# Performance work log

Hardware: AMD Instinct MI355X
Metric: run time of the kernel (lower is better)

Reference implementation:

```python
import jax, jax.numpy as jnp
import numpy as np

EMB = 1024
HEADS = 16
HEAD_DIM = EMB // HEADS
FF = 4 * EMB
B, S = 4, 2048


def gelu_tanh(x):
    c = jnp.sqrt(jnp.asarray(2.0 / jnp.pi, x.dtype))
    return 0.5 * x * (1.0 + jnp.tanh(c * (x + 0.044715 * x ** 3)))


def layernorm(x, g, b, eps=1e-5):
    mu = jnp.mean(x, axis=-1, keepdims=True)
    var = jnp.var(x, axis=-1, keepdims=True)
    return (x - mu) * jax.lax.rsqrt(var + eps) * g + b


def setup_inputs() -> dict:
    key = jax.random.key(0)
    ks = jax.random.split(key, 12)
    s = 0.02
    return {
        "x": jax.random.normal(ks[0], (B, S, EMB), jnp.float32),
        "Wq": jax.random.normal(ks[1], (EMB, EMB), jnp.float32) * s,
        "bq": jnp.zeros((EMB,), jnp.float32),
        "Wk": jax.random.normal(ks[2], (EMB, EMB), jnp.float32) * s,
        "bk": jnp.zeros((EMB,), jnp.float32),
        "Wv": jax.random.normal(ks[3], (EMB, EMB), jnp.float32) * s,
        "bv": jnp.zeros((EMB,), jnp.float32),
        "Wo": jax.random.normal(ks[4], (EMB, EMB), jnp.float32) * s,
        "bo": jnp.zeros((EMB,), jnp.float32),
        "W1": jax.random.normal(ks[5], (EMB, FF), jnp.float32) * s,
        "b1": jnp.zeros((FF,), jnp.float32),
        "W2": jax.random.normal(ks[6], (FF, EMB), jnp.float32) * s,
        "b2": jnp.zeros((EMB,), jnp.float32),
        "g1": jnp.ones((EMB,), jnp.float32),
        "be1": jnp.zeros((EMB,), jnp.float32),
        "g2": jnp.ones((EMB,), jnp.float32),
        "be2": jnp.zeros((EMB,), jnp.float32),
    }


def reference(x, Wq, bq, Wk, bk, Wv, bv, Wo, bo, W1, b1, W2, b2, g1, be1, g2, be2):
    b, s, _ = x.shape
    shortcut = x
    h = layernorm(x, g1, be1)
    # QKV projections -> [b, heads, s, head_dim]
    def proj(W, bias):
        return (h @ W + bias).reshape(b, s, HEADS, HEAD_DIM).transpose(0, 2, 1, 3)
    q, k, v = proj(Wq, bq), proj(Wk, bk), proj(Wv, bv)
    scores = jnp.einsum('bhqd,bhkd->bhqk', q, k) / jnp.sqrt(jnp.asarray(HEAD_DIM, x.dtype))
    causal = jnp.triu(jnp.ones((s, s), bool), k=1)  # True above diagonal -> masked
    scores = jnp.where(causal, -jnp.inf, scores)
    probs = jax.nn.softmax(scores, axis=-1)  # dropout p=0 -> identity
    ctx = jnp.einsum('bhqk,bhkd->bhqd', probs, v).transpose(0, 2, 1, 3).reshape(b, s, EMB)
    attn_out = ctx @ Wo + bo
    x = attn_out + shortcut
    shortcut = x
    h = layernorm(x, g2, be2)
    ff = gelu_tanh(h @ W1 + b1) @ W2 + b2
    return ff + shortcut
```

## Files before the change

### kernel.cpp

```cpp
#include <hip/hip_runtime.h>
#include <hip/hip_bf16.h>

#define EMB 1024
#define HEADS 16
#define HDIM 64
#define FFDIM 4096
#define BSZ 4
#define SEQ 2048
#define MROWS (BSZ * SEQ)
#define QKVW 3072
#define VSTRIDE 2080

typedef __attribute__((ext_vector_type(8))) short bf16x8;
typedef __attribute__((ext_vector_type(4))) float f32x4;
typedef __attribute__((ext_vector_type(16))) float f32x16;
typedef __attribute__((ext_vector_type(4))) unsigned short u16x4;
typedef unsigned short u16;

__device__ __forceinline__ float bf2f(u16 u) {
  union { unsigned int i; float f; } c; c.i = ((unsigned int)u) << 16; return c.f;
}
__device__ __forceinline__ u16 f2bf(float f) {
  union { float f; unsigned int i; } c; c.f = f;
  unsigned int i = c.i + 0x7fff + ((c.i >> 16) & 1);
  return (u16)(i >> 16);
}
__device__ __forceinline__ unsigned fbits(float f) {
  union { float f; unsigned u; } c; c.f = f; return c.u;
}
__device__ __forceinline__ unsigned pk2(float e0, float e1) {
  return (fbits(e0) >> 16) | (fbits(e1) & 0xffff0000u);
}
__device__ __forceinline__ f32x16 zero16() {
  f32x16 z;
#pragma unroll
  for (int i = 0; i < 16; ++i) z[i] = 0.f;
  return z;
}
__device__ __forceinline__ void gload16(const u16* g, void* lds) {
  __builtin_amdgcn_global_load_lds(
      (const __attribute__((address_space(1))) void*)g,
      (__attribute__((address_space(3))) void*)lds, 16, 0, 0);
}

__global__ __launch_bounds__(256) void ln_kernel(
    const float* __restrict__ x, const float* __restrict__ g,
    const float* __restrict__ be, u16* __restrict__ out) {
  int w = threadIdx.x >> 6, l = threadIdx.x & 63;
  size_t row = (size_t)blockIdx.x * 4 + w;
  const float* xr = x + row * EMB;
  float f[4][4];
  float s = 0.f, s2 = 0.f;
#pragma unroll
  for (int c = 0; c < 4; ++c) {
    f32x4 v = *(const f32x4*)(xr + c * 256 + l * 4);
#pragma unroll
    for (int j = 0; j < 4; ++j) {
      f[c][j] = v[j];
      s += v[j];
      s2 += v[j] * v[j];
    }
  }
#pragma unroll
  for (int m = 1; m < 64; m <<= 1) {
    s  += __shfl_xor(s, m);
    s2 += __shfl_xor(s2, m);
  }
  float mu = s * (1.f / EMB);
  float var = s2 * (1.f / EMB) - mu * mu;
  float rs = rsqrtf(var + 1e-5f);
#pragma unroll
  for (int c = 0; c < 4; ++c) {
    u16x4 o;
#pragma unroll
    for (int j = 0; j < 4; ++j) {
      int col = c * 256 + l * 4 + j;
      o[j] = f2bf((f[c][j] - mu) * rs * g[col] + be[col]);
    }
    *(u16x4*)(out + row * EMB + c * 256 + l * 4) = o;
  }
}

__global__ __launch_bounds__(256) void transpose_cvt(
    const float* __restrict__ in, u16* __restrict__ out, int R, int C) {
  __shared__ u16 tile[32][33];
  int c0 = blockIdx.x * 32, r0 = blockIdx.y * 32;
  int tx = threadIdx.x, ty = threadIdx.y;
#pragma unroll
  for (int i = ty; i < 32; i += 8)
    tile[i][tx] = f2bf(in[(size_t)(r0 + i) * C + c0 + tx]);
  __syncthreads();
#pragma unroll
  for (int i = ty; i < 32; i += 8)
    out[(size_t)(c0 + i) * R + r0 + tx] = tile[tx][i];
}

__global__ __launch_bounds__(256) void concat_bias(
    const float* __restrict__ a, const float* __restrict__ b,
    const float* __restrict__ c, float* __restrict__ o) {
  int i = blockIdx.x * 256 + threadIdx.x;
  o[i] = i < 1024 ? a[i] : (i < 2048 ? b[i - 1024] : c[i - 2048]);
}

__global__ __launch_bounds__(256) void transpose_v(
    const u16* __restrict__ QKV, u16* __restrict__ Vt) {
  __shared__ u16 tile[32][33];
  int s0 = blockIdx.x * 32, d0 = blockIdx.y * 32, bh = blockIdx.z;
  int h = bh % HEADS, b = bh / HEADS;
  int tx = threadIdx.x, ty = threadIdx.y;
  const u16* src = QKV + (size_t)b * SEQ * QKVW + 2048 + h * HDIM;
  u16* dst = Vt + (size_t)bh * HDIM * VSTRIDE;
#pragma unroll
  for (int i = ty; i < 32; i += 8)
    tile[i][tx] = src[(size_t)(s0 + i) * QKVW + d0 + tx];
  __syncthreads();
#pragma unroll
  for (int i = ty; i < 32; i += 8)
    dst[(size_t)(d0 + i) * VSTRIDE + s0 + tx] = tile[tx][i];
}

__device__ __forceinline__ float gelu_f(float v) {
  float inner = 0.7978845608028654f * (v + 0.044715f * v * v * v);
  return 0.5f * v * (1.f + tanhf(inner));
}

template <int MFR, int EPI, typename OT>
__global__ __launch_bounds__(512, 1) void gemm_p(
    const u16* __restrict__ A, const u16* __restrict__ Bt,
    const float* __restrict__ bias, const float* __restrict__ res,
    OT* __restrict__ C, int N, int K) {
  constexpr int BM = MFR * 32;
  constexpr int HHALF = (BM + 256) * 32;
  constexpr int NA = MFR / 2;
  constexpr int LPH = NA + 2;
  __shared__ u16 lds[4 * HHALF];
  int nbn = N >> 8;
  int cpx = gridDim.x >> 3;
  int bid = blockIdx.x;
  int logical = (bid & 7) * cpx + (bid >> 3);
  int mb = logical / nbn, nb = logical % nbn;
  int m0 = mb * BM, n0 = nb << 8;
  int t = threadIdx.x, w = t >> 6, l = t & 63;
  int lg = l >> 4, lc = l & 15;
  int wr = w >> 2, wc = w & 3;
  int NT = K >> 6, NH = NT * 2;
  f32x4 acc[MFR][4] = {};

  auto stage = [&](int H) {
    int kb = (H >> 1) * 64 + (H & 1) * 32;
    char* hb = (char*)lds + (H & 3) * (HHALF * 2);
#pragma unroll
    for (int i = 0; i < NA; ++i) {
      int q = i * 512 + t;
      int r = q >> 2, p = q & 3;
      int kc = kb + ((p ^ ((r >> 1) & 3)) << 3);
      gload16(A + (size_t)(m0 + r) * K + kc, hb + i * 8192 + w * 1024);
    }
#pragma unroll
    for (int i = 0; i < 2; ++i) {
      int q = i * 512 + t;
      int r = q >> 2, p = q & 3;
      int kc = kb + ((p ^ ((r >> 1) & 3)) << 3);
      gload16(Bt + (size_t)(n0 + r) * K + kc, hb + BM * 64 + i * 8192 + w * 1024);
    }
  };

  stage(0); stage(1); stage(2); stage(3);
  if constexpr (LPH == 4) asm volatile("s_waitcnt vmcnt(8)" ::: "memory");
  else                    asm volatile("s_waitcnt vmcnt(6)" ::: "memory");
  __builtin_amdgcn_s_barrier();
  __builtin_amdgcn_sched_barrier(0);

  for (int h = 0; h < NH; ++h) {
    const u16* lb = lds + (h & 3) * HHALF;
    bf16x8 bfr[4], afr[MFR];
#pragma unroll
    for (int n = 0; n < 4; ++n) {
      int rb = (wc << 6) + (n << 4) + lc;
      bfr[n] = *(const bf16x8*)(lb + BM * 32 + rb * 32 + ((lg ^ ((rb >> 1) & 3)) << 3));
    }
#pragma unroll
    for (int m = 0; m < MFR; ++m) {
      int ra = wr * (MFR * 16) + (m << 4) + lc;
      afr[m] = *(const bf16x8*)(lb + ra * 32 + ((lg ^ ((ra >> 1) & 3)) << 3));
    }
    __builtin_amdgcn_s_setprio(1);
#pragma unroll
    for (int m = 0; m < MFR; ++m)
#pragma unroll
      for (int n = 0; n < 4; ++n)
        acc[m][n] = __builtin_amdgcn_mfma_f32_16x16x32_bf16(
            afr[m], bfr[n], acc[m][n], 0, 0, 0);
    __builtin_amdgcn_s_setprio(0);
    if (h < NH - 1) {
      int rem = NH - 2 - h;
      if (rem >= 2) {
        if constexpr (LPH == 4) asm volatile("s_waitcnt vmcnt(8)" ::: "memory");
        else                    asm volatile("s_waitcnt vmcnt(6)" ::: "memory");
      } else if (rem == 1) {
        if constexpr (LPH == 4) asm volatile("s_waitcnt vmcnt(4)" ::: "memory");
        else                    asm volatile("s_waitcnt vmcnt(3)" ::: "memory");
      } else {
        asm volatile("s_waitcnt vmcnt(0)" ::: "memory");
      }
      __builtin_amdgcn_s_barrier();
      __builtin_amdgcn_sched_barrier(0);
      if (h + 4 < NH) stage(h + 4);
    }
  }

#pragma unroll
  for (int m = 0; m < MFR; ++m)
#pragma unroll
    for (int n = 0; n < 4; ++n) {
      int col = n0 + (wc << 6) + (n << 4) + lc;
      float bcol = bias[col];
#pragma unroll
      for (int r = 0; r < 4; ++r) {
        int row = m0 + wr * (MFR * 16) + (m << 4) + (lg << 2) + r;
        float v = acc[m][n][r] + bcol;
        if (EPI & 2) v = gelu_f(v);
        if (EPI & 1) v += res[(size_t)row * N + col];
        if (sizeof(OT) == 2)
          C[(size_t)row * N + col] = (OT)f2bf(v);
        else
          C[(size_t)row * N + col] = (OT)v;
      }
    }
}

#define QKT32(ACCS, QF)                                                     \
  do {                                                                      \
    ACCS = zero16();                                                        \
    _Pragma("unroll") for (int s_ = 0; s_ < 4; ++s_)                        \
        ACCS = __builtin_amdgcn_mfma_f32_32x32x16_bf16(kf[s_], QF[s_],      \
                                                       ACCS, 0, 0, 0);      \
  } while (0)

#define ATTN_STEP(ACCS, M, L, O0, O1, DIAG)                                 \
  do {                                                                      \
    float e_[16];                                                           \
    float tm = -1e30f;                                                      \
    _Pragma("unroll") for (int i = 0; i < 16; ++i) {                        \
      float sv = ACCS[i];                                                   \
      if (DIAG) {                                                           \
        int kvl = (i & 3) + 8 * (i >> 2) + 4 * g;                           \
        if (kvl > lq) sv = -1e30f;                                          \
      }                                                                     \
      e_[i] = sv;                                                           \
      tm = fmaxf(tm, sv);                                                   \
    }                                                                       \
    tm = fmaxf(tm, __shfl_xor(tm, 32));                                     \
    float nm = fmaxf(M, tm);                                                \
    if (!__all(tm <= M)) {                                                  \
      float scl = __expf(M - nm);                                           \
      L *= scl;                                                             \
      _Pragma("unroll") for (int i = 0; i < 16; ++i) {                      \
        O0[i] *= scl;                                                       \
        O1[i] *= scl;                                                       \
      }                                                                     \
    }                                                                       \
    M = nm;                                                                 \
    float ts = 0.f;                                                         \
    _Pragma("unroll") for (int i = 0; i < 16; ++i) {                        \
      e_[i] = __expf(e_[i] - nm);                                           \
      ts += e_[i];                                                          \
    }                                                                       \
    ts += __shfl_xor(ts, 32);                                               \
    L += ts;                                                                \
    _Pragma("unroll") for (int s_ = 0; s_ < 2; ++s_) {                      \
      unsigned plo0 = pk2(e_[8 * s_ + 0], e_[8 * s_ + 1]);                  \
      unsigned plo1 = pk2(e_[8 * s_ + 2], e_[8 * s_ + 3]);                  \
      unsigned phi0 = pk2(e_[8 * s_ + 4], e_[8 * s_ + 5]);                  \
      unsigned phi1 = pk2(e_[8 * s_ + 6], e_[8 * s_ + 7]);                  \
      unsigned recv0 = __shfl_xor(g ? plo0 : phi0, 32);                     \
      unsigned recv1 = __shfl_xor(g ? plo1 : phi1, 32);                     \
      union { unsigned u[4]; bf16x8 v; } pf_;                               \
      pf_.u[0] = g ? recv0 : plo0;                                          \
      pf_.u[1] = g ? recv1 : plo1;                                          \
      pf_.u[2] = g ? phi0 : recv0;                                          \
      pf_.u[3] = g ? phi1 : recv1;                                          \
      O0 = __builtin_amdgcn_mfma_f32_32x32x16_bf16(vf[0][s_], pf_.v, O0,    \
                                                   0, 0, 0);                \
      O1 = __builtin_amdgcn_mfma_f32_32x32x16_bf16(vf[1][s_], pf_.v, O1,    \
                                                   0, 0, 0);                \
    }                                                                       \
  } while (0)

#define LOAD_KV(KV0)                                                        \
  do {                                                                      \
    _Pragma("unroll") for (int s_ = 0; s_ < 4; ++s_)                        \
        kf[s_] = *(const bf16x8*)(Kp + (size_t)((KV0) + lq) * QKVW +        \
                                  s_ * 16 + g * 8);                         \
    _Pragma("unroll") for (int d_ = 0; d_ < 2; ++d_)                        \
        _Pragma("unroll") for (int s_ = 0; s_ < 2; ++s_)                    \
            vf[d_][s_] = *(const bf16x8*)(Vt +                              \
                (size_t)(d_ * 32 + lq) * VSTRIDE + (KV0) + s_ * 16 + g * 8);\
  } while (0)

#define WRITE_OUT(O0, O1, L, WQ0)                                           \
  do {                                                                      \
    float inv = 1.f / L;                                                    \
    u16* orow = Op + (size_t)((WQ0) + lq) * EMB;                            \
    _Pragma("unroll") for (int dblk = 0; dblk < 2; ++dblk) {                \
      _Pragma("unroll") for (int p = 0; p < 8; ++p) {                       \
        int i0 = 2 * p;                                                     \
        int d = dblk * 32 + 2 * (p & 1) + 8 * (p >> 1) + 4 * g;             \
        float v0 = (dblk ? O1[i0] : O0[i0]) * inv;                          \
        float v1 = (dblk ? O1[i0 + 1] : O0[i0 + 1]) * inv;                  \
        unsigned wd = (unsigned)f2bf(v0) | ((unsigned)f2bf(v1) << 16);      \
        *(unsigned*)(orow + d) = wd;                                        \
      }                                                                     \
    }                                                                       \
  } while (0)

__global__ __launch_bounds__(256, 2) void attn_kernel(
    const u16* __restrict__ QKV, const u16* __restrict__ VtG,
    u16* __restrict__ O) {
  int t = threadIdx.x, w = t >> 6, l = t & 63;
  int lq = l & 31, g = l >> 5;
  int wid = blockIdx.x * 4 + w;
  int qi = wid & 31, bh = wid >> 5;
  int h = bh & (HEADS - 1), b = bh >> 4;
  int wq0a = qi * 32, wq0b = (63 - qi) * 32;
  int ntA = qi + 1, ntB = 64 - qi;
  const u16* Qp = QKV + (size_t)b * SEQ * QKVW + h * HDIM;
  const u16* Kp = QKV + (size_t)b * SEQ * QKVW + 1024 + h * HDIM;
  const u16* Vt = VtG + (size_t)bh * HDIM * VSTRIDE;
  u16* Op = O + (size_t)b * SEQ * EMB + h * HDIM;

  bf16x8 qfA[4], qfB[4];
#pragma unroll
  for (int s = 0; s < 4; ++s) {
    bf16x8 ra = *(const bf16x8*)(Qp + (size_t)(wq0a + lq) * QKVW + s * 16 + g * 8);
    bf16x8 rb = *(const bf16x8*)(Qp + (size_t)(wq0b + lq) * QKVW + s * 16 + g * 8);
#pragma unroll
    for (int j = 0; j < 8; ++j) {
      qfA[s][j] = (short)f2bf(bf2f((u16)ra[j]) * 0.125f);
      qfB[s][j] = (short)f2bf(bf2f((u16)rb[j]) * 0.125f);
    }
  }

  f32x16 oA0 = zero16(), oA1 = zero16(), oB0 = zero16(), oB1 = zero16();
  f32x16 sA, sB;
  float mA = -1e30f, lA = 0.f, mB = -1e30f, lB = 0.f;
  bf16x8 kf[4], vf[2][2];

  for (int ti = 0; ti < ntA; ++ti) {
    int kv0 = ti * 32;
    LOAD_KV(kv0);
    QKT32(sA, qfA);
    QKT32(sB, qfB);
    bool diagA = (ti == ntA - 1);
    ATTN_STEP(sA, mA, lA, oA0, oA1, diagA);
    ATTN_STEP(sB, mB, lB, oB0, oB1, false);
  }
  WRITE_OUT(oA0, oA1, lA, wq0a);
  for (int ti = ntA; ti < ntB; ++ti) {
    int kv0 = ti * 32;
    LOAD_KV(kv0);
    QKT32(sB, qfB);
    bool diagB = (ti == ntB - 1);
    ATTN_STEP(sB, mB, lB, oB0, oB1, diagB);
  }
  WRITE_OUT(oB0, oB1, lB, wq0b);
}

extern "C" void kernel_launch(void* const* d_in, const int* in_sizes, int n_in,
                              void* d_out, int out_size, void* d_ws, size_t ws_size,
                              hipStream_t stream) {
  (void)in_sizes; (void)n_in; (void)out_size; (void)ws_size;
  const float* x   = (const float*)d_in[0];
  const float* Wq  = (const float*)d_in[1];
  const float* bq  = (const float*)d_in[2];
  const float* Wk  = (const float*)d_in[3];
  const float* bk  = (const float*)d_in[4];
  const float* Wv  = (const float*)d_in[5];
  const float* bv  = (const float*)d_in[6];
  const float* Wo  = (const float*)d_in[7];
  const float* bo  = (const float*)d_in[8];
  const float* W1  = (const float*)d_in[9];
  const float* b1  = (const float*)d_in[10];
  const float* W2  = (const float*)d_in[11];
  const float* b2  = (const float*)d_in[12];
  const float* g1  = (const float*)d_in[13];
  const float* be1 = (const float*)d_in[14];
  const float* g2  = (const float*)d_in[15];
  const float* be2 = (const float*)d_in[16];

  char* ws = (char*)d_ws;
  const size_t MB = 1ull << 20;
  u16*   WqkvT = (u16*)(ws + 0 * MB);
  u16*   WoT   = (u16*)(ws + 6 * MB);
  u16*   W1T   = (u16*)(ws + 8 * MB);
  u16*   W2T   = (u16*)(ws + 16 * MB);
  float* bqkv  = (float*)(ws + 24 * MB);
  u16*   hbuf  = (u16*)(ws + 25 * MB);
  float* x1f   = (float*)(ws + 41 * MB);
  u16*   qkv   = (u16*)(ws + 73 * MB);
  u16*   VtG   = (u16*)(ws + 121 * MB);
  u16*   gbuf  = (u16*)(ws + 73 * MB);

  dim3 tb(32, 8);
  transpose_cvt<<<dim3(EMB / 32, EMB / 32), tb, 0, stream>>>(Wq, WqkvT, EMB, EMB);
  transpose_cvt<<<dim3(EMB / 32, EMB / 32), tb, 0, stream>>>(Wk, WqkvT + 1024 * 1024, EMB, EMB);
  transpose_cvt<<<dim3(EMB / 32, EMB / 32), tb, 0, stream>>>(Wv, WqkvT + 2 * 1024 * 1024, EMB, EMB);
  transpose_cvt<<<dim3(EMB / 32, EMB / 32), tb, 0, stream>>>(Wo, WoT, EMB, EMB);
  transpose_cvt<<<dim3(FFDIM / 32, EMB / 32), tb, 0, stream>>>(W1, W1T, EMB, FFDIM);
  transpose_cvt<<<dim3(EMB / 32, FFDIM / 32), tb, 0, stream>>>(W2, W2T, FFDIM, EMB);
  concat_bias<<<12, 256, 0, stream>>>(bq, bk, bv, bqkv);

  ln_kernel<<<MROWS / 4, 256, 0, stream>>>(x, g1, be1, hbuf);

  gemm_p<8, 0, u16><<<(MROWS / 256) * (QKVW / 256), 512, 0, stream>>>(
      hbuf, WqkvT, bqkv, nullptr, qkv, QKVW, EMB);

  transpose_v<<<dim3(SEQ / 32, HDIM / 32, BSZ * HEADS), tb, 0, stream>>>(qkv, VtG);

  attn_kernel<<<BSZ * HEADS * (SEQ / 64) / 4, 256, 0, stream>>>(qkv, VtG, hbuf);

  gemm_p<4, 1, float><<<(MROWS / 128) * (EMB / 256), 512, 0, stream>>>(
      hbuf, WoT, bo, x, x1f, EMB, EMB);

  ln_kernel<<<MROWS / 4, 256, 0, stream>>>(x1f, g2, be2, hbuf);

  gemm_p<8, 2, u16><<<(MROWS / 256) * (FFDIM / 256), 512, 0, stream>>>(
      hbuf, W1T, b1, nullptr, gbuf, FFDIM, EMB);
  gemm_p<4, 1, float><<<(MROWS / 128) * (EMB / 256), 512, 0, stream>>>(
      gbuf, W2T, b2, x1f, (float*)d_out, EMB, FFDIM);
}
```

Before: 474.2 us.

## Restructure GEMM pipeline into split A/B staging with two-phase MFMA per k-tile

Replaces the half-tile 4-stage GEMM with a k-tile (32-wide) 4-slot ring where A and B global loads are issued separately, interleaved between two MFMA phases that each cover half of the M fragments. LDS fragment reads for the second half overlap the first phase's math, and extra barriers plus lgkmcnt waits enforce ordering. The intent is better overlap of global loads, LDS reads and MFMA. In exchange it adds more barriers per iteration, and the swizzle/wait accounting must exactly match the new load counts.

```diff
diff --git a/kernel.cpp b/kernel.cpp
--- a/kernel.cpp
+++ b/kernel.cpp
@@ -124,16 +124,16 @@
   return 0.5f * v * (1.f + tanhf(inner));
 }
 
-template <int MFR, int EPI, typename OT>
-__global__ __launch_bounds__(512, 1) void gemm_p(
+template <int MQ, int EPI, typename OT>
+__global__ __launch_bounds__(512, 1) void gemm_t(
     const u16* __restrict__ A, const u16* __restrict__ Bt,
     const float* __restrict__ bias, const float* __restrict__ res,
     OT* __restrict__ C, int N, int K) {
-  constexpr int BM = MFR * 32;
-  constexpr int HHALF = (BM + 256) * 32;
-  constexpr int NA = MFR / 2;
-  constexpr int LPH = NA + 2;
-  __shared__ u16 lds[4 * HHALF];
+  constexpr int BM = MQ * 64;
+  constexpr int NA = BM / 128;
+  constexpr int LPT = NA + 2;
+  constexpr int SLOTB = BM * 64 + 16384;
+  __shared__ char ldsb[4 * SLOTB];
   int nbn = N >> 8;
   int cpx = gridDim.x >> 3;
   int bid = blockIdx.x;
@@ -143,81 +143,111 @@
   int t = threadIdx.x, w = t >> 6, l = t & 63;
   int lg = l >> 4, lc = l & 15;
   int wr = w >> 2, wc = w & 3;
-  int NT = K >> 6, NH = NT * 2;
-  f32x4 acc[MFR][4] = {};
-
-  auto stage = [&](int H) {
-    int kb = (H >> 1) * 64 + (H & 1) * 32;
-    char* hb = (char*)lds + (H & 3) * (HHALF * 2);
+  int NT = K >> 5;
+  int swsrc = ((l & 3) ^ ((l >> 3) & 3)) << 3;
+  int lrow = l >> 2;
+
+  f32x4 acc[MQ * 2][4] = {};
+
+  auto stageA = [&](int kt) {
+    char* sb = ldsb + (kt & 3) * SLOTB;
 #pragma unroll
     for (int i = 0; i < NA; ++i) {
-      int q = i * 512 + t;
-      int r = q >> 2, p = q & 3;
-      int kc = kb + ((p ^ ((r >> 1) & 3)) << 3);
-      gload16(A + (size_t)(m0 + r) * K + kc, hb + i * 8192 + w * 1024);
-    }
+      int row0 = w * (BM / 8) + i * 16;
+      gload16(A + (size_t)(m0 + row0 + lrow) * K + kt * 32 + swsrc,
+              sb + row0 * 64);
+    }
+  };
+  auto stageB = [&](int kt) {
+    char* sb = ldsb + (kt & 3) * SLOTB + BM * 64;
 #pragma unroll
     for (int i = 0; i < 2; ++i) {
-      int q = i * 512 + t;
-      int r = q >> 2, p = q & 3;
-      int kc = kb + ((p ^ ((r >> 1) & 3)) << 3);
-      gload16(Bt + (size_t)(n0 + r) * K + kc, hb + BM * 64 + i * 8192 + w * 1024);
+      int row0 = w * 32 + i * 16;
+      gload16(Bt + (size_t)(n0 + row0 + lrow) * K + kt * 32 + swsrc,
+              sb + row0 * 64);
     }
   };
 
-  stage(0); stage(1); stage(2); stage(3);
-  if constexpr (LPH == 4) asm volatile("s_waitcnt vmcnt(8)" ::: "memory");
-  else                    asm volatile("s_waitcnt vmcnt(6)" ::: "memory");
+  stageA(0); stageB(0); stageA(1); stageB(1); stageA(2); stageB(2);
+  asm volatile("s_waitcnt vmcnt(%0)" :: "i"(2 * LPT) : "memory");
   __builtin_amdgcn_s_barrier();
-  __builtin_amdgcn_sched_barrier(0);
-
-  for (int h = 0; h < NH; ++h) {
-    const u16* lb = lds + (h & 3) * HHALF;
-    bf16x8 bfr[4], afr[MFR];
+
+  for (int kt = 0; kt < NT; ++kt) {
+    const char* sb = ldsb + (kt & 3) * SLOTB;
+    bf16x8 bfr[4];
 #pragma unroll
     for (int n = 0; n < 4; ++n) {
-      int rb = (wc << 6) + (n << 4) + lc;
-      bfr[n] = *(const bf16x8*)(lb + BM * 32 + rb * 32 + ((lg ^ ((rb >> 1) & 3)) << 3));
-    }
-#pragma unroll
-    for (int m = 0; m < MFR; ++m) {
-      int ra = wr * (MFR * 16) + (m << 4) + lc;
-      afr[m] = *(const bf16x8*)(lb + ra * 32 + ((lg ^ ((ra >> 1) & 3)) << 3));
-    }
+      int row = wc * 64 + n * 16 + lc;
+      bfr[n] = *(const bf16x8*)(sb + BM * 64 + row * 64 +
+                                ((lg ^ ((row >> 1) & 3)) << 4));
+    }
+    bf16x8 af0[MQ / 2][2];
+#pragma unroll
+    for (int j = 0; j < MQ / 2; ++j)
+#pragma unroll
+      for (int s = 0; s < 2; ++s) {
+        int row = wr * (MQ * 32) + j * 32 + s * 16 + lc;
+        af0[j][s] = *(const bf16x8*)(sb + row * 64 +
+                                     ((lg ^ ((row >> 1) & 3)) << 4));
+      }
+    if (kt + 3 < NT) stageA(kt + 3);
+    __builtin_amdgcn_s_barrier();
+    asm volatile("s_waitcnt lgkmcnt(0)" ::: "memory");
+    __builtin_amdgcn_sched_barrier(0);
     __builtin_amdgcn_s_setprio(1);
 #pragma unroll
-    for (int m = 0; m < MFR; ++m)
-#pragma unroll
-      for (int n = 0; n < 4; ++n)
-        acc[m][n] = __builtin_amdgcn_mfma_f32_16x16x32_bf16(
-            afr[m], bfr[n], acc[m][n], 0, 0, 0);
+    for (int j = 0; j < MQ / 2; ++j)
+#pragma unroll
+      for (int s = 0; s < 2; ++s)
+#pragma unroll
+        for (int n = 0; n < 4; ++n)
+          acc[j * 2 + s][n] = __builtin_amdgcn_mfma_f32_16x16x32_bf16(
+              af0[j][s], bfr[n], acc[j * 2 + s][n], 0, 0, 0);
     __builtin_amdgcn_s_setprio(0);
-    if (h < NH - 1) {
-      int rem = NH - 2 - h;
-      if (rem >= 2) {
-        if constexpr (LPH == 4) asm volatile("s_waitcnt vmcnt(8)" ::: "memory");
-        else                    asm volatile("s_waitcnt vmcnt(6)" ::: "memory");
-      } else if (rem == 1) {
-        if constexpr (LPH == 4) asm volatile("s_waitcnt vmcnt(4)" ::: "memory");
-        else                    asm volatile("s_waitcnt vmcnt(3)" ::: "memory");
-      } else {
-        asm volatile("s_waitcnt vmcnt(0)" ::: "memory");
+    __builtin_amdgcn_s_barrier();
+    bf16x8 af1[MQ / 2][2];
+#pragma unroll
+    for (int j = 0; j < MQ / 2; ++j)
+#pragma unroll
+      for (int s = 0; s < 2; ++s) {
+        int row = wr * (MQ * 32) + (MQ / 2 + j) * 32 + s * 16 + lc;
+        af1[j][s] = *(const bf16x8*)(sb + row * 64 +
+                                     ((lg ^ ((row >> 1) & 3)) << 4));
       }
-      __builtin_amdgcn_s_barrier();
-      __builtin_amdgcn_sched_barrier(0);
-      if (h + 4 < NH) stage(h + 4);
-    }
-  }
-
-#pragma unroll
-  for (int m = 0; m < MFR; ++m)
+    if (kt + 3 < NT) stageB(kt + 3);
+    int rem = NT - 1 - kt;
+    if (rem >= 3)
+      asm volatile("s_waitcnt vmcnt(%0)" :: "i"(2 * LPT) : "memory");
+    else if (rem == 2)
+      asm volatile("s_waitcnt vmcnt(%0)" :: "i"(LPT) : "memory");
+    else if (rem == 1)
+      asm volatile("s_waitcnt vmcnt(0)" ::: "memory");
+    __builtin_amdgcn_s_barrier();
+    asm volatile("s_waitcnt lgkmcnt(0)" ::: "memory");
+    __builtin_amdgcn_sched_barrier(0);
+    __builtin_amdgcn_s_setprio(1);
+#pragma unroll
+    for (int j = 0; j < MQ / 2; ++j)
+#pragma unroll
+      for (int s = 0; s < 2; ++s)
+#pragma unroll
+        for (int n = 0; n < 4; ++n)
+          acc[(MQ / 2 + j) * 2 + s][n] =
+              __builtin_amdgcn_mfma_f32_16x16x32_bf16(
+                  af1[j][s], bfr[n], acc[(MQ / 2 + j) * 2 + s][n], 0, 0, 0);
+    __builtin_amdgcn_s_setprio(0);
+    __builtin_amdgcn_s_barrier();
+  }
+
+#pragma unroll
+  for (int m = 0; m < MQ * 2; ++m)
 #pragma unroll
     for (int n = 0; n < 4; ++n) {
       int col = n0 + (wc << 6) + (n << 4) + lc;
       float bcol = bias[col];
 #pragma unroll
       for (int r = 0; r < 4; ++r) {
-        int row = m0 + wr * (MFR * 16) + (m << 4) + (lg << 2) + r;
+        int row = m0 + wr * (MQ * 32) + (m << 4) + (lg << 2) + r;
         float v = acc[m][n][r] + bcol;
         if (EPI & 2) v = gelu_f(v);
         if (EPI & 1) v += res[(size_t)row * N + col];
@@ -412,20 +442,20 @@
 
   ln_kernel<<<MROWS / 4, 256, 0, stream>>>(x, g1, be1, hbuf);
 
-  gemm_p<8, 0, u16><<<(MROWS / 256) * (QKVW / 256), 512, 0, stream>>>(
+  gemm_t<4, 0, u16><<<(MROWS / 256) * (QKVW / 256), 512, 0, stream>>>(
       hbuf, WqkvT, bqkv, nullptr, qkv, QKVW, EMB);
 
   transpose_v<<<dim3(SEQ / 32, HDIM / 32, BSZ * HEADS), tb, 0, stream>>>(qkv, VtG);
 
   attn_kernel<<<BSZ * HEADS * (SEQ / 64) / 4, 256, 0, stream>>>(qkv, VtG, hbuf);
 
-  gemm_p<4, 1, float><<<(MROWS / 128) * (EMB / 256), 512, 0, stream>>>(
+  gemm_t<2, 1, float><<<(MROWS / 128) * (EMB / 256), 512, 0, stream>>>(
       hbuf, WoT, bo, x, x1f, EMB, EMB);
 
   ln_kernel<<<MROWS / 4, 256, 0, stream>>>(x1f, g2, be2, hbuf);
 
-  gemm_p<8, 2, u16><<<(MROWS / 256) * (FFDIM / 256), 512, 0, stream>>>(
+  gemm_t<4, 2, u16><<<(MROWS / 256) * (FFDIM / 256), 512, 0, stream>>>(
       hbuf, W1T, b1, nullptr, gbuf, FFDIM, EMB);
-  gemm_p<4, 1, float><<<(MROWS / 128) * (EMB / 256), 512, 0, stream>>>(
+  gemm_t<2, 1, float><<<(MROWS / 128) * (EMB / 256), 512, 0, stream>>>(
       gbuf, W2T, b2, x1f, (float*)d_out, EMB, FFDIM);
 }
```

New measurement: 471.9 us. About the same (-0.5%).

## Replace pipelined 16x16 GEMM with single-buffered 128x128 32x32-MFMA GEMM

Applied to the files above, without the earlier changes.

Replaces the 512-thread, 4-stage LDS-pipelined GEMM (256-wide N tiles, 16x16x32 MFMA) with a simpler 256-thread kernel. The new kernel uses 128x128 tiles, a single 16KB LDS buffer, 32x32x16 MFMA and occupancy of 3 blocks per CU. The aim is to rely on multiple resident blocks to hide latency instead of software pipelining, and to use the larger MFMA shape. The GELU is also rewritten as a sigmoid form with __expf. The risk is losing the prefetch overlap, since each k-step does load, sync and compute serially, and the smaller tiles reduce data reuse.

```diff
diff --git a/kernel.cpp b/kernel.cpp
--- a/kernel.cpp
+++ b/kernel.cpp
@@ -120,105 +120,72 @@
 }
 
 __device__ __forceinline__ float gelu_f(float v) {
-  float inner = 0.7978845608028654f * (v + 0.044715f * v * v * v);
-  return 0.5f * v * (1.f + tanhf(inner));
-}
-
-template <int MFR, int EPI, typename OT>
-__global__ __launch_bounds__(512, 1) void gemm_p(
+  float u = 1.5957691216057308f * (v + 0.044715f * v * v * v);
+  return v / (1.f + __expf(-u));
+}
+
+template <int EPI, typename OT>
+__global__ __launch_bounds__(256, 3) void gemm32(
     const u16* __restrict__ A, const u16* __restrict__ Bt,
     const float* __restrict__ bias, const float* __restrict__ res,
     OT* __restrict__ C, int N, int K) {
-  constexpr int BM = MFR * 32;
-  constexpr int HHALF = (BM + 256) * 32;
-  constexpr int NA = MFR / 2;
-  constexpr int LPH = NA + 2;
-  __shared__ u16 lds[4 * HHALF];
-  int nbn = N >> 8;
+  __shared__ char lds[16384];
+  int nbn = N >> 7;
   int cpx = gridDim.x >> 3;
   int bid = blockIdx.x;
   int logical = (bid & 7) * cpx + (bid >> 3);
   int mb = logical / nbn, nb = logical % nbn;
-  int m0 = mb * BM, n0 = nb << 8;
+  int m0 = mb << 7, n0 = nb << 7;
   int t = threadIdx.x, w = t >> 6, l = t & 63;
-  int lg = l >> 4, lc = l & 15;
-  int wr = w >> 2, wc = w & 3;
-  int NT = K >> 6, NH = NT * 2;
-  f32x4 acc[MFR][4] = {};
-
-  auto stage = [&](int H) {
-    int kb = (H >> 1) * 64 + (H & 1) * 32;
-    char* hb = (char*)lds + (H & 3) * (HHALF * 2);
-#pragma unroll
-    for (int i = 0; i < NA; ++i) {
-      int q = i * 512 + t;
-      int r = q >> 2, p = q & 3;
-      int kc = kb + ((p ^ ((r >> 1) & 3)) << 3);
-      gload16(A + (size_t)(m0 + r) * K + kc, hb + i * 8192 + w * 1024);
-    }
-#pragma unroll
-    for (int i = 0; i < 2; ++i) {
-      int q = i * 512 + t;
-      int r = q >> 2, p = q & 3;
-      int kc = kb + ((p ^ ((r >> 1) & 3)) << 3);
-      gload16(Bt + (size_t)(n0 + r) * K + kc, hb + BM * 64 + i * 8192 + w * 1024);
-    }
-  };
-
-  stage(0); stage(1); stage(2); stage(3);
-  if constexpr (LPH == 4) asm volatile("s_waitcnt vmcnt(8)" ::: "memory");
-  else                    asm volatile("s_waitcnt vmcnt(6)" ::: "memory");
-  __builtin_amdgcn_s_barrier();
-  __builtin_amdgcn_sched_barrier(0);
-
-  for (int h = 0; h < NH; ++h) {
-    const u16* lb = lds + (h & 3) * HHALF;
-    bf16x8 bfr[4], afr[MFR];
-#pragma unroll
-    for (int n = 0; n < 4; ++n) {
-      int rb = (wc << 6) + (n << 4) + lc;
-      bfr[n] = *(const bf16x8*)(lb + BM * 32 + rb * 32 + ((lg ^ ((rb >> 1) & 3)) << 3));
-    }
-#pragma unroll
-    for (int m = 0; m < MFR; ++m) {
-      int ra = wr * (MFR * 16) + (m << 4) + lc;
-      afr[m] = *(const bf16x8*)(lb + ra * 32 + ((lg ^ ((ra >> 1) & 3)) << 3));
-    }
-    __builtin_amdgcn_s_setprio(1);
-#pragma unroll
-    for (int m = 0; m < MFR; ++m)
-#pragma unroll
-      for (int n = 0; n < 4; ++n)
-        acc[m][n] = __builtin_amdgcn_mfma_f32_16x16x32_bf16(
-            afr[m], bfr[n], acc[m][n], 0, 0, 0);
-    __builtin_amdgcn_s_setprio(0);
-    if (h < NH - 1) {
-      int rem = NH - 2 - h;
-      if (rem >= 2) {
-        if constexpr (LPH == 4) asm volatile("s_waitcnt vmcnt(8)" ::: "memory");
-        else                    asm volatile("s_waitcnt vmcnt(6)" ::: "memory");
-      } else if (rem == 1) {
-        if constexpr (LPH == 4) asm volatile("s_waitcnt vmcnt(4)" ::: "memory");
-        else                    asm volatile("s_waitcnt vmcnt(3)" ::: "memory");
-      } else {
-        asm volatile("s_waitcnt vmcnt(0)" ::: "memory");
+  int wr = w >> 1, wc = w & 1;
+  int l31 = l & 31, lh = l >> 5;
+  int srow = (w << 4) + (l >> 2);
+  int scol = (((l & 3) ^ ((srow >> 1) & 3)) << 3);
+  char* dstA = lds + (w << 10);
+  char* dstB = lds + 8192 + (w << 10);
+
+  f32x16 acc[2][2] = {{zero16(), zero16()}, {zero16(), zero16()}};
+
+  for (int k0 = 0; k0 < K; k0 += 32) {
+    __syncthreads();
+    gload16(A + (size_t)(m0 + srow) * K + k0 + scol, dstA);
+    gload16(A + (size_t)(m0 + 64 + srow) * K + k0 + scol, dstA + 4096);
+    gload16(Bt + (size_t)(n0 + srow) * K + k0 + scol, dstB);
+    gload16(Bt + (size_t)(n0 + 64 + srow) * K + k0 + scol, dstB + 4096);
+    __syncthreads();
+    bf16x8 afr[2][2], bfr[2][2];
+#pragma unroll
+    for (int blk = 0; blk < 2; ++blk)
+#pragma unroll
+      for (int kk = 0; kk < 2; ++kk) {
+        int ra = (wr << 6) + (blk << 5) + l31;
+        int rb = (wc << 6) + (blk << 5) + l31;
+        int pa = (((kk << 1) + lh) ^ ((ra >> 1) & 3)) << 4;
+        int pb = (((kk << 1) + lh) ^ ((rb >> 1) & 3)) << 4;
+        afr[blk][kk] = *(const bf16x8*)(lds + ra * 64 + pa);
+        bfr[blk][kk] = *(const bf16x8*)(lds + 8192 + rb * 64 + pb);
       }
-      __builtin_amdgcn_s_barrier();
-      __builtin_amdgcn_sched_barrier(0);
-      if (h + 4 < NH) stage(h + 4);
-    }
-  }
-
-#pragma unroll
-  for (int m = 0; m < MFR; ++m)
-#pragma unroll
-    for (int n = 0; n < 4; ++n) {
-      int col = n0 + (wc << 6) + (n << 4) + lc;
+#pragma unroll
+    for (int m = 0; m < 2; ++m)
+#pragma unroll
+      for (int n = 0; n < 2; ++n)
+#pragma unroll
+        for (int kk = 0; kk < 2; ++kk)
+          acc[m][n] = __builtin_amdgcn_mfma_f32_32x32x16_bf16(
+              afr[m][kk], bfr[n][kk], acc[m][n], 0, 0, 0);
+  }
+
+#pragma unroll
+  for (int m = 0; m < 2; ++m)
+#pragma unroll
+    for (int n = 0; n < 2; ++n) {
+      int col = n0 + (wc << 6) + (n << 5) + l31;
       float bcol = bias[col];
-#pragma unroll
-      for (int r = 0; r < 4; ++r) {
-        int row = m0 + wr * (MFR * 16) + (m << 4) + (lg << 2) + r;
-        float v = acc[m][n][r] + bcol;
+      int rbase = m0 + (wr << 6) + (m << 5) + (lh << 2);
+#pragma unroll
+      for (int reg = 0; reg < 16; ++reg) {
+        int row = rbase + (reg & 3) + ((reg >> 2) << 3);
+        float v = acc[m][n][reg] + bcol;
         if (EPI & 2) v = gelu_f(v);
         if (EPI & 1) v += res[(size_t)row * N + col];
         if (sizeof(OT) == 2)
@@ -412,20 +379,20 @@
 
   ln_kernel<<<MROWS / 4, 256, 0, stream>>>(x, g1, be1, hbuf);
 
-  gemm_p<8, 0, u16><<<(MROWS / 256) * (QKVW / 256), 512, 0, stream>>>(
+  gemm32<0, u16><<<(MROWS / 128) * (QKVW / 128), 256, 0, stream>>>(
       hbuf, WqkvT, bqkv, nullptr, qkv, QKVW, EMB);
 
   transpose_v<<<dim3(SEQ / 32, HDIM / 32, BSZ * HEADS), tb, 0, stream>>>(qkv, VtG);
 
   attn_kernel<<<BSZ * HEADS * (SEQ / 64) / 4, 256, 0, stream>>>(qkv, VtG, hbuf);
 
-  gemm_p<4, 1, float><<<(MROWS / 128) * (EMB / 256), 512, 0, stream>>>(
+  gemm32<1, float><<<(MROWS / 128) * (EMB / 128), 256, 0, stream>>>(
       hbuf, WoT, bo, x, x1f, EMB, EMB);
 
   ln_kernel<<<MROWS / 4, 256, 0, stream>>>(x1f, g2, be2, hbuf);
 
-  gemm_p<8, 2, u16><<<(MROWS / 256) * (FFDIM / 256), 512, 0, stream>>>(
+  gemm32<2, u16><<<(MROWS / 128) * (FFDIM / 128), 256, 0, stream>>>(
       hbuf, W1T, b1, nullptr, gbuf, FFDIM, EMB);
-  gemm_p<4, 1, float><<<(MROWS / 128) * (EMB / 256), 512, 0, stream>>>(
+  gemm32<1, float><<<(MROWS / 128) * (EMB / 128), 256, 0, stream>>>(
       gbuf, W2T, b2, x1f, (float*)d_out, EMB, FFDIM);
 }
```

Measured after the change: 454.1 us. -4.2%, faster.
